# Kernel tuning notes

Measured on AMD Instinct MI355X. Metric: run time of the kernel, lower is better.

The kernel has to match this reference:

```python
import jax, jax.numpy as jnp
import numpy as np

N_NODES = 20000
N_EDGES = 320000
EMB = 256
K_DIFF = 3
BN_EPS = 1e-5


def conv1d(x, w, b, stride):
    # x: [N, Cin, L], w: [Cout, Cin, K]
    y = jax.lax.conv_general_dilated(x, w, window_strides=(stride,), padding='VALID',
                                     dimension_numbers=('NCH', 'OIH', 'NCH'))
    return y + b[None, :, None]


def batchnorm_train(x, gamma, beta):
    # training-mode BatchNorm1d over (N, L) per channel, biased variance
    m = jnp.mean(x, axis=(0, 2), keepdims=True)
    v = jnp.var(x, axis=(0, 2), keepdims=True)
    return (x - m) * jax.lax.rsqrt(v + BN_EPS) * gamma[None, :, None] + beta[None, :, None]


def dconv(X, W, b, row, col, norm_out, norm_in, n):
    # Diffusion convolution (pytorch_geometric_temporal DConv), K hops,
    # forward (out-degree) and backward (in-degree) random walks.
    def prop(x, norm):
        msg = norm[:, None] * x[row]                    # [E, F] gather
        return jax.ops.segment_sum(msg, col, num_segments=n)  # scatter-add to targets

    K = W.shape[1]
    Tx_0 = X
    Tx_1 = X
    H = X @ W[0, 0] + X @ W[1, 0]
    if K > 1:
        Tx_1_o = prop(X, norm_out)
        Tx_1_i = prop(X, norm_in)
        H = H + Tx_1_o @ W[0, 1] + Tx_1_i @ W[1, 1]
    for k in range(2, K):
        Tx_2_o = 2.0 * prop(Tx_1_o, norm_out) - Tx_0
        Tx_2_i = 2.0 * prop(Tx_1_i, norm_in) - Tx_0
        H = H + Tx_2_o @ W[0, k] + Tx_2_i @ W[1, k]
        Tx_0, Tx_1_o, Tx_1_i = Tx_1, Tx_2_o, Tx_2_i
    return H + b


def setup_inputs() -> dict:
    key = jax.random.key(0)
    ks = jax.random.split(key, 16)
    d_in = 2 * EMB  # concat([X, H])
    inp = {
        'x': jax.random.normal(ks[0], (N_NODES, 1, 100), dtype=jnp.float32),
        'edge_index': jax.random.randint(ks[1], (2, N_EDGES), 0, N_NODES, dtype=jnp.int32),
        'hidden_state': jax.random.normal(ks[2], (N_NODES, EMB), dtype=jnp.float32),
        'conv1_w': jax.random.normal(ks[3], (32, 1, 10), dtype=jnp.float32) * 0.2,
        'conv1_b': jnp.zeros((32,), jnp.float32),
        'bn1_gamma': jnp.ones((32,), jnp.float32),
        'bn1_beta': jnp.zeros((32,), jnp.float32),
        'conv2_w': jax.random.normal(ks[4], (32, 32, 10), dtype=jnp.float32) * 0.05,
        'conv2_b': jnp.zeros((32,), jnp.float32),
        'bn2_gamma': jnp.ones((32,), jnp.float32),
        'bn2_beta': jnp.zeros((32,), jnp.float32),
        'W_z': jax.random.normal(ks[5], (2, K_DIFF, d_in, EMB), dtype=jnp.float32) * 0.05,
        'b_z': jnp.zeros((EMB,), jnp.float32),
        'W_r': jax.random.normal(ks[6], (2, K_DIFF, d_in, EMB), dtype=jnp.float32) * 0.05,
        'b_r': jnp.zeros((EMB,), jnp.float32),
        'W_h': jax.random.normal(ks[7], (2, K_DIFF, d_in, EMB), dtype=jnp.float32) * 0.05,
        'b_h': jnp.zeros((EMB,), jnp.float32),
    }
    return inp


def reference(x, edge_index, hidden_state, conv1_w, conv1_b, bn1_gamma, bn1_beta,
              conv2_w, conv2_b, bn2_gamma, bn2_beta, W_z, b_z, W_r, b_r, W_h, b_h):
    n = x.shape[0]
    # CNN embedding: conv -> relu -> bn, twice
    h = batchnorm_train(jax.nn.relu(conv1d(x, conv1_w, conv1_b, 3)), bn1_gamma, bn1_beta)
    h = batchnorm_train(jax.nn.relu(conv1d(h, conv2_w, conv2_b, 3)), bn2_gamma, bn2_beta)
    X = h.reshape(n, -1)  # [N, EMB]

    row, col = edge_index[0], edge_index[1]
    ones = jnp.ones((row.shape[0],), X.dtype)
    deg_out = jax.ops.segment_sum(ones, row, num_segments=n)
    deg_in = jax.ops.segment_sum(ones, col, num_segments=n)
    norm_out = (1.0 / deg_out)[row]
    norm_in = (1.0 / deg_in)[col]

    H0 = hidden_state
    XH = jnp.concatenate([X, H0], axis=1)
    Z = jax.nn.sigmoid(dconv(XH, W_z, b_z, row, col, norm_out, norm_in, n))
    R = jax.nn.sigmoid(dconv(XH, W_r, b_r, row, col, norm_out, norm_in, n))
    XRH = jnp.concatenate([X, R * H0], axis=1)
    H_tilde = jnp.tanh(dconv(XRH, W_h, b_h, row, col, norm_out, norm_in, n))
    H = Z * H0 + (1.0 - Z) * H_tilde
    return jax.nn.relu(H)
```

## Files before the change

kernel.cpp:

```cpp
#include <hip/hip_runtime.h>
#include <cstdint>
#include <cstddef>

#define NN 20000
#define NE 320000

typedef float f32x4 __attribute__((ext_vector_type(4)));
typedef short s16x8 __attribute__((ext_vector_type(8)));
typedef unsigned short us;

struct KBd { const us* p; int rs; int cs; };
struct KB10 { KBd b[10]; };

__device__ __forceinline__ us f2bf(float x){
    unsigned u = __float_as_uint(x);
    unsigned r = (u + 0x7fffu + ((u >> 16) & 1u)) >> 16;
    return (us)r;
}
__device__ __forceinline__ float bf2f(us s){
    return __uint_as_float(((unsigned)s) << 16);
}

__device__ __forceinline__ void gl16(const void* g, void* l){
    __builtin_amdgcn_global_load_lds((const __attribute__((address_space(1))) unsigned int*)g,
                                     (__attribute__((address_space(3))) unsigned int*)l, 16, 0, 0);
}

__device__ __forceinline__ void upd8(uint4 v, float w, float* ao, float* ai){
    float f0=__uint_as_float(v.x<<16), f1=__uint_as_float(v.x&0xffff0000u);
    float f2=__uint_as_float(v.y<<16), f3=__uint_as_float(v.y&0xffff0000u);
    float f4=__uint_as_float(v.z<<16), f5=__uint_as_float(v.z&0xffff0000u);
    float f6=__uint_as_float(v.w<<16), f7=__uint_as_float(v.w&0xffff0000u);
    ao[0]=fmaf(w,f0,ao[0]); ao[1]=fmaf(w,f1,ao[1]); ao[2]=fmaf(w,f2,ao[2]); ao[3]=fmaf(w,f3,ao[3]);
    ao[4]=fmaf(w,f4,ao[4]); ao[5]=fmaf(w,f5,ao[5]); ao[6]=fmaf(w,f6,ao[6]); ao[7]=fmaf(w,f7,ao[7]);
    ai[0]+=f0; ai[1]+=f1; ai[2]+=f2; ai[3]+=f3; ai[4]+=f4; ai[5]+=f5; ai[6]+=f6; ai[7]+=f7;
}
__device__ __forceinline__ void updw(uint4 v, float w, float* a){
    float f0=__uint_as_float(v.x<<16), f1=__uint_as_float(v.x&0xffff0000u);
    float f2=__uint_as_float(v.y<<16), f3=__uint_as_float(v.y&0xffff0000u);
    float f4=__uint_as_float(v.z<<16), f5=__uint_as_float(v.z&0xffff0000u);
    float f6=__uint_as_float(v.w<<16), f7=__uint_as_float(v.w&0xffff0000u);
    a[0]=fmaf(w,f0,a[0]); a[1]=fmaf(w,f1,a[1]); a[2]=fmaf(w,f2,a[2]); a[3]=fmaf(w,f3,a[3]);
    a[4]=fmaf(w,f4,a[4]); a[5]=fmaf(w,f5,a[5]); a[6]=fmaf(w,f6,a[6]); a[7]=fmaf(w,f7,a[7]);
}
__device__ __forceinline__ uint4 pack8(const float* a){
    uint4 r;
    r.x=((unsigned)f2bf(a[1])<<16)|f2bf(a[0]);
    r.y=((unsigned)f2bf(a[3])<<16)|f2bf(a[2]);
    r.z=((unsigned)f2bf(a[5])<<16)|f2bf(a[4]);
    r.w=((unsigned)f2bf(a[7])<<16)|f2bf(a[6]);
    return r;
}
__device__ __forceinline__ uint4 pack8s(const float* a, float s){
    uint4 r;
    r.x=((unsigned)f2bf(s*a[1])<<16)|f2bf(s*a[0]);
    r.y=((unsigned)f2bf(s*a[3])<<16)|f2bf(s*a[2]);
    r.z=((unsigned)f2bf(s*a[5])<<16)|f2bf(s*a[4]);
    r.w=((unsigned)f2bf(s*a[7])<<16)|f2bf(s*a[6]);
    return r;
}


__global__ void k_zero(uint32_t* p, int n){
    int i = blockIdx.x*256 + threadIdx.x;
    if(i < n) p[i] = 0u;
}

__global__ void k_degree(const int* __restrict__ ei, int* degout, int* degin){
    int e = blockIdx.x*256 + threadIdx.x;
    if(e < NE){
        atomicAdd(&degout[ei[e]], 1);
        atomicAdd(&degin[ei[NE+e]], 1);
    }
}

__global__ void k_scan(const int* __restrict__ degin, int* __restrict__ coloff,
                       float* __restrict__ invdegin){
    __shared__ int part[1024];
    int t = threadIdx.x;
    int base = t*20;
    int s = 0;
    for(int k=0;k<20;k++){ int i = base+k; if(i < NN) s += degin[i]; }
    part[t] = s;
    __syncthreads();
    for(int off=1; off<1024; off<<=1){
        int v = (t>=off) ? part[t-off] : 0;
        __syncthreads();
        part[t] += v;
        __syncthreads();
    }
    int run = (t>0) ? part[t-1] : 0;
    for(int k=0;k<20;k++){
        int i = base+k;
        if(i < NN){
            int d = degin[i];
            coloff[i] = run;
            run += d;
            invdegin[i] = (d>0) ? (1.0f/(float)d) : 0.0f;
        }
    }
    if(t==1023) coloff[NN] = part[1023];
}

__global__ void k_csr(const int* __restrict__ ei, const int* __restrict__ degout,
                      const int* __restrict__ coloff, int* cnt, int2* __restrict__ ew){
    int e = blockIdx.x*256 + threadIdx.x;
    if(e < NE){
        int r = ei[e], c = ei[NE+e];
        int pos = coloff[c] + atomicAdd(&cnt[c], 1);
        int2 v; v.x = r; v.y = __float_as_int(1.0f/(float)degout[r]);
        ew[pos] = v;
    }
}


__global__ void k_conv1(const float* __restrict__ x, const float* __restrict__ w1,
                        const float* __restrict__ b1, us* __restrict__ y1b){
    __shared__ float w[320];
    __shared__ float bb[32];
    int t = threadIdx.x;
    for(int i=t;i<320;i+=256) w[i] = w1[i];
    if(t < 32) bb[t] = b1[t];
    __syncthreads();
    int gid = blockIdx.x*256 + t;
    if(gid >= NN*31) return;
    int node = gid/31, p = gid - node*31;
    const float* xr = x + node*100 + 3*p;
    float xv[10];
    #pragma unroll
    for(int k=0;k<10;k++) xv[k] = xr[k];
    us* yo = y1b + (size_t)node*1024 + p;
    #pragma unroll
    for(int c=0;c<32;c++){
        float a = bb[c];
        #pragma unroll
        for(int k=0;k<10;k++) a = fmaf(w[c*10+k], xv[k], a);
        yo[c*32] = f2bf(fmaxf(a, 0.0f));
    }
    if(p == 0){
        #pragma unroll
        for(int c=0;c<32;c++) y1b[(size_t)node*1024 + c*32 + 31] = 0;
    }
}

template<int SLOTS, int PPC>
__global__ void k_chanstats_bf(const us* __restrict__ y, float* __restrict__ sq){
    int tid = blockIdx.x*blockDim.x + threadIdx.x;
    int slot = tid & (SLOTS-1);
    int node0 = tid / SLOTS;
    int nstride = (gridDim.x*blockDim.x) / SLOTS;
    int c = slot / PPC;
    float s = 0.f, q = 0.f;
    for(int n=node0; n<NN; n+=nstride){
        float v = bf2f(y[(size_t)n*SLOTS + slot]);
        s += v; q = fmaf(v, v, q);
    }
    #pragma unroll
    for(int m=PPC>>1; m>0; m>>=1){
        s += __shfl_xor(s, m);
        q += __shfl_xor(q, m);
    }
    if((threadIdx.x & (PPC-1)) == 0){
        atomicAdd(&sq[c], s);
        atomicAdd(&sq[32+c], q);
    }
}

__global__ void k_bnfin(const float* __restrict__ sq, const float* __restrict__ gamma,
                        const float* __restrict__ beta, float* __restrict__ scsh,
                        float inv_count){
    int c = threadIdx.x;
    if(c < 32){
        float m = sq[c]*inv_count;
        float v = sq[32+c]*inv_count - m*m;
        float sc = gamma[c]*rsqrtf(v + 1e-5f);
        scsh[c] = sc;
        scsh[32+c] = beta[c] - m*sc;
    }
}

__global__ void __launch_bounds__(256) k_conv2(const us* __restrict__ y1b,
                        const float* __restrict__ w2, const float* __restrict__ b2,
                        const float* __restrict__ scsh1, us* __restrict__ Xpre){
    __shared__ float wlds[10240];
    __shared__ float hlds[8*1040];
    int t = threadIdx.x;
    int node0 = blockIdx.x*8;
    #pragma unroll
    for(int j=0;j<40;j++){
        int idx = j*256 + t;
        int ck = idx>>5, c2 = idx&31;
        wlds[ck*32 + c2] = w2[c2*320 + ck];
    }
    #pragma unroll
    for(int j=0;j<32;j++){
        int idx = j*256 + t;
        int nl = idx>>10, i = idx&1023;
        int c = i>>5;
        hlds[nl*1040 + i] = fmaf(scsh1[c], bf2f(y1b[(size_t)(node0+nl)*1024 + i]), scsh1[32+c]);
    }
    __syncthreads();
    int nl = t>>5, c2 = t&31;
    int hbase = nl*1040;
    float acc[8];
    float b = b2[c2];
    #pragma unroll
    for(int p=0;p<8;p++) acc[p] = b;
    for(int c=0;c<32;c++){
        float wr[10];
        #pragma unroll
        for(int k=0;k<10;k++) wr[k] = wlds[(c*10+k)*32 + c2];
        float hv[32];
        #pragma unroll
        for(int q=0;q<8;q++){
            float4 v = *(const float4*)&hlds[hbase + c*32 + q*4];
            hv[q*4+0]=v.x; hv[q*4+1]=v.y; hv[q*4+2]=v.z; hv[q*4+3]=v.w;
        }
        #pragma unroll
        for(int p=0;p<8;p++){
            #pragma unroll
            for(int k=0;k<10;k++)
                acc[p] = fmaf(wr[k], hv[3*p+k], acc[p]);
        }
    }
    uint4 pk;
    pk.x = ((unsigned)f2bf(fmaxf(acc[1],0.f))<<16) | f2bf(fmaxf(acc[0],0.f));
    pk.y = ((unsigned)f2bf(fmaxf(acc[3],0.f))<<16) | f2bf(fmaxf(acc[2],0.f));
    pk.z = ((unsigned)f2bf(fmaxf(acc[5],0.f))<<16) | f2bf(fmaxf(acc[4],0.f));
    pk.w = ((unsigned)f2bf(fmaxf(acc[7],0.f))<<16) | f2bf(fmaxf(acc[6],0.f));
    *(uint4*)&Xpre[(size_t)(node0+nl)*256 + c2*8] = pk;
}

__global__ void __launch_bounds__(256) k_prep(const us* __restrict__ Xpre,
        const float* __restrict__ scsh, const float* __restrict__ h0,
        us* __restrict__ XHp){
    int node = blockIdx.x*4 + (threadIdx.x>>6);
    if(node >= NN) return;
    int lane = threadIdx.x & 63;
    int half = lane>>5, g = lane&31;
    uint4 o;
    if(half == 0){
        uint4 v = *(const uint4*)(Xpre + (size_t)node*256 + g*8);
        float sc = scsh[g], sh = scsh[32+g];
        float y[8];
        y[0]=fmaf(sc,__uint_as_float(v.x<<16),sh); y[1]=fmaf(sc,__uint_as_float(v.x&0xffff0000u),sh);
        y[2]=fmaf(sc,__uint_as_float(v.y<<16),sh); y[3]=fmaf(sc,__uint_as_float(v.y&0xffff0000u),sh);
        y[4]=fmaf(sc,__uint_as_float(v.z<<16),sh); y[5]=fmaf(sc,__uint_as_float(v.z&0xffff0000u),sh);
        y[6]=fmaf(sc,__uint_as_float(v.w<<16),sh); y[7]=fmaf(sc,__uint_as_float(v.w&0xffff0000u),sh);
        o = pack8(y);
    }else{
        float4 a = *(const float4*)(h0 + (size_t)node*256 + g*8);
        float4 b = *(const float4*)(h0 + (size_t)node*256 + g*8 + 4);
        float y[8] = {a.x,a.y,a.z,a.w,b.x,b.y,b.z,b.w};
        o = pack8(y);
    }
    *(uint4*)(XHp + (size_t)node*512 + (size_t)g*16 + half*8) = o;
}


__device__ __forceinline__ float weff_val(const float* W, int term, size_t base){
    const size_t S = 512*256;
    if(term==0)      return W[0*S+base] + W[3*S+base] - W[2*S+base] - W[5*S+base];
    else if(term==1) return W[1*S+base];
    else if(term==2) return W[4*S+base];
    else if(term==3) return 2.0f*W[2*S+base];
    else             return 2.0f*W[5*S+base];
}

__global__ void k_weff_zr_t(const float* __restrict__ Wz, const float* __restrict__ Wr,
                            us* __restrict__ Wt){
    int k = blockIdx.x*256 + threadIdx.x;
    int col = blockIdx.y;
    const float* W = (col < 256) ? Wz : Wr;
    int j = col & 255;
    int kb = k >> 8, rr = k & 255;
    size_t base = (size_t)((kb & 1)*256 + rr)*256 + j;
    Wt[(size_t)col*2560 + k] = f2bf(weff_val(W, kb>>1, base));
}

__global__ void k_weff_h_t(const float* __restrict__ Wh, us* __restrict__ Wt){
    int k = blockIdx.x*256 + threadIdx.x;
    int col = blockIdx.y;
    int kb = k >> 8, rr = k & 255;
    size_t base = (size_t)((kb & 1)*256 + rr)*256 + col;
    Wt[(size_t)col*2560 + k] = f2bf(weff_val(Wh, kb>>1, base));
}


__global__ void __launch_bounds__(256) k_prop1(const us* __restrict__ XHp,
        const int* __restrict__ coloff, const int2* __restrict__ ew,
        const float* __restrict__ invdeg, us* __restrict__ T1op, us* __restrict__ T1ip){
    int node = blockIdx.x*4 + (threadIdx.x>>6);
    if(node >= NN) return;
    int lane = threadIdx.x & 63;
    size_t lo = (size_t)(lane&31)*16 + (lane>>5)*8;
    int s = coloff[node], e = coloff[node+1];
    float ao[8]={0,0,0,0,0,0,0,0}, ai[8]={0,0,0,0,0,0,0,0};
    int j = s;
    for(; j+3 < e; j += 4){
        int2 e0=ew[j], e1=ew[j+1], e2=ew[j+2], e3=ew[j+3];
        uint4 v0=*(const uint4*)(XHp+(size_t)e0.x*512+lo);
        uint4 v1=*(const uint4*)(XHp+(size_t)e1.x*512+lo);
        uint4 v2=*(const uint4*)(XHp+(size_t)e2.x*512+lo);
        uint4 v3=*(const uint4*)(XHp+(size_t)e3.x*512+lo);
        upd8(v0,__int_as_float(e0.y),ao,ai);
        upd8(v1,__int_as_float(e1.y),ao,ai);
        upd8(v2,__int_as_float(e2.y),ao,ai);
        upd8(v3,__int_as_float(e3.y),ao,ai);
    }
    for(; j < e; j++){
        int2 ed = ew[j];
        uint4 v = *(const uint4*)(XHp+(size_t)ed.x*512+lo);
        upd8(v,__int_as_float(ed.y),ao,ai);
    }
    float wi = invdeg[node];
    *(uint4*)(T1op+(size_t)node*512+lo) = pack8(ao);
    *(uint4*)(T1ip+(size_t)node*512+lo) = pack8s(ai,wi);
}

__global__ void __launch_bounds__(256) k_prop2(const us* __restrict__ T1op,
        const us* __restrict__ T1ip,
        const int* __restrict__ coloff, const int2* __restrict__ ew,
        const float* __restrict__ invdeg, us* __restrict__ P2op, us* __restrict__ P2ip){
    int node = blockIdx.x*4 + (threadIdx.x>>6);
    if(node >= NN) return;
    int lane = threadIdx.x & 63;
    size_t lo = (size_t)(lane&31)*16 + (lane>>5)*8;
    int s = coloff[node], e = coloff[node+1];
    float ao[8]={0,0,0,0,0,0,0,0}, ai[8]={0,0,0,0,0,0,0,0};
    int j = s;
    for(; j+1 < e; j += 2){
        int2 e0=ew[j], e1=ew[j+1];
        size_t o0=(size_t)e0.x*512+lo, o1=(size_t)e1.x*512+lo;
        uint4 a0=*(const uint4*)(T1op+o0), b0=*(const uint4*)(T1ip+o0);
        uint4 a1=*(const uint4*)(T1op+o1), b1=*(const uint4*)(T1ip+o1);
        float one = 1.0f;
        updw(a0,__int_as_float(e0.y),ao); updw(b0,one,ai);
        updw(a1,__int_as_float(e1.y),ao); updw(b1,one,ai);
    }
    if(j < e){
        int2 ed = ew[j];
        size_t o0=(size_t)ed.x*512+lo;
        uint4 a0=*(const uint4*)(T1op+o0), b0=*(const uint4*)(T1ip+o0);
        updw(a0,__int_as_float(ed.y),ao); updw(b0,1.0f,ai);
    }
    float wi = invdeg[node];
    *(uint4*)(P2op+(size_t)node*512+lo) = pack8(ao);
    *(uint4*)(P2ip+(size_t)node*512+lo) = pack8s(ai,wi);
}

__global__ void __launch_bounds__(256) k_propq1(const us* __restrict__ RHb,
        const int* __restrict__ coloff, const int2* __restrict__ ew,
        const float* __restrict__ invdeg, us* __restrict__ Q1p){
    int node = blockIdx.x*4 + (threadIdx.x>>6);
    if(node >= NN) return;
    int lane = threadIdx.x & 63;
    int half = lane>>5, g = lane&31;
    int s = coloff[node], e = coloff[node+1];
    float ao[8]={0,0,0,0,0,0,0,0}, ai[8]={0,0,0,0,0,0,0,0};
    int j = s;
    for(; j+1 < e; j += 2){
        int2 ed = ew[j+half];
        uint4 v = *(const uint4*)(RHb+(size_t)ed.x*256+g*8);
        upd8(v,__int_as_float(ed.y),ao,ai);
    }
    if(j < e && half == 0){
        int2 ed = ew[j];
        uint4 v = *(const uint4*)(RHb+(size_t)ed.x*256+g*8);
        upd8(v,__int_as_float(ed.y),ao,ai);
    }
    #pragma unroll
    for(int k=0;k<8;k++){
        ao[k] += __shfl_xor(ao[k],32);
        ai[k] += __shfl_xor(ai[k],32);
    }
    if(half == 0){
        float wi = invdeg[node];
        *(uint4*)(Q1p+(size_t)node*512+(size_t)g*16)   = pack8(ao);
        *(uint4*)(Q1p+(size_t)node*512+(size_t)g*16+8) = pack8s(ai,wi);
    }
}

__global__ void __launch_bounds__(256) k_propq2(const us* __restrict__ Q1p,
        const int* __restrict__ coloff, const int2* __restrict__ ew,
        const float* __restrict__ invdeg, us* __restrict__ Q2p){
    int node = blockIdx.x*4 + (threadIdx.x>>6);
    if(node >= NN) return;
    int lane = threadIdx.x & 63;
    int half = lane>>5;
    size_t lo = (size_t)(lane&31)*16 + half*8;
    int s = coloff[node], e = coloff[node+1];
    float a[8]={0,0,0,0,0,0,0,0};
    int j = s;
    for(; j+3 < e; j += 4){
        int2 e0=ew[j], e1=ew[j+1], e2=ew[j+2], e3=ew[j+3];
        uint4 v0=*(const uint4*)(Q1p+(size_t)e0.x*512+lo);
        uint4 v1=*(const uint4*)(Q1p+(size_t)e1.x*512+lo);
        uint4 v2=*(const uint4*)(Q1p+(size_t)e2.x*512+lo);
        uint4 v3=*(const uint4*)(Q1p+(size_t)e3.x*512+lo);
        updw(v0, half ? 1.0f : __int_as_float(e0.y), a);
        updw(v1, half ? 1.0f : __int_as_float(e1.y), a);
        updw(v2, half ? 1.0f : __int_as_float(e2.y), a);
        updw(v3, half ? 1.0f : __int_as_float(e3.y), a);
    }
    for(; j < e; j++){
        int2 ed = ew[j];
        uint4 v = *(const uint4*)(Q1p+(size_t)ed.x*512+lo);
        updw(v, half ? 1.0f : __int_as_float(ed.y), a);
    }
    float sc = half ? invdeg[node] : 1.0f;
    *(uint4*)(Q2p+(size_t)node*512+lo) = pack8s(a,sc);
}


template<int MODE, int BNT>
__global__ void __launch_bounds__(256) k_gemm(KB10 blocks, const us* __restrict__ Wt,
        const float* __restrict__ bias0, const float* __restrict__ bias1,
        const float* __restrict__ h0, const float* __restrict__ Zin,
        float* __restrict__ out0, us* __restrict__ out1){
    constexpr int WN = BNT/32;
    constexpr int NB = BNT/64;
    __shared__ us As[2][4096];
    __shared__ us Bs[2][BNT*32];
    int t = threadIdx.x;
    int wid = t >> 6, lane = t & 63;
    int l15 = lane & 15, kg = lane >> 4;

    int bid = blockIdx.x;
    int xcd = bid & 7, sblk = bid >> 3;
    int cidx = sblk & 3, r = (sblk >> 2)*8 + xcd;
    if(r >= 157) return;
    int row0 = r*128, col0 = cidx*BNT;
    int rowbase = (wid >> 1)*64, colbase = (wid & 1)*(BNT/2);
    int swz = (l15 >> 1) & 3;

    int srA[2], sgA[2], graA[2];
    #pragma unroll
    for(int i=0;i<2;i++){
        int c = t + i*256;
        srA[i] = c >> 2;
        sgA[i] = (c & 3) ^ ((srA[i] >> 1) & 3);
        int gr = row0 + srA[i];
        graA[i] = (gr < NN) ? gr : NN-1;
    }
    int srB[NB], sgB[NB];
    #pragma unroll
    for(int i=0;i<NB;i++){
        int c = t + i*256;
        srB[i] = c >> 2;
        sgB[i] = (c & 3) ^ ((srB[i] >> 1) & 3);
    }

    f32x4 acc[4][WN] = {};

    auto stage = [&](int buf, int step){
        int kb = step >> 3, kt = (step & 7)*32, ktc = (step & 7)*4;
        const us* Ap = blocks.b[kb].p;
        int rs = blocks.b[kb].rs, cs = blocks.b[kb].cs;
        #pragma unroll
        for(int i=0;i<2;i++)
            gl16(Ap + (size_t)graA[i]*rs + (size_t)(ktc + sgA[i])*cs, &As[buf][(t+i*256)*8]);
        const us* Wp = Wt + (size_t)kb*256;
        #pragma unroll
        for(int i=0;i<NB;i++)
            gl16(Wp + (size_t)(col0+srB[i])*2560 + kt + sgB[i]*8, &Bs[buf][(t+i*256)*8]);
    };

    stage(0, 0);
    __syncthreads();
    int cur = 0;
    for(int step=0; step<80; step++){
        if(step < 79) stage(cur^1, step+1);
        s16x8 af[4], bfr[WN];
        #pragma unroll
        for(int i=0;i<4;i++){
            int row = rowbase + i*16 + l15;
            af[i] = *(const s16x8*)&As[cur][(row*4 + (kg ^ swz))*8];
        }
        #pragma unroll
        for(int n=0;n<WN;n++){
            int colr = colbase + n*16 + l15;
            bfr[n] = *(const s16x8*)&Bs[cur][(colr*4 + (kg ^ swz))*8];
        }
        #pragma unroll
        for(int mi=0;mi<4;mi++){
            #pragma unroll
            for(int ni=0;ni<WN;ni++){
                acc[mi][ni] = __builtin_amdgcn_mfma_f32_16x16x32_bf16(
                    af[mi], bfr[ni], acc[mi][ni], 0, 0, 0);
            }
        }
        __syncthreads();
        cur ^= 1;
    }

    #pragma unroll
    for(int mi=0;mi<4;mi++){
        int gr0 = row0 + rowbase + mi*16 + kg*4;
        #pragma unroll
        for(int ni=0;ni<WN;ni++){
            int j = col0 + colbase + ni*16 + l15;
            #pragma unroll
            for(int rr=0;rr<4;rr++){
                int gr = gr0 + rr;
                if(gr < NN){
                    float a = acc[mi][ni][rr];
                    if(MODE == 0){
                        if(j < 256){
                            out0[(size_t)gr*256 + j] = 1.0f/(1.0f + expf(-(a + bias0[j])));
                        }else{
                            int jj = j - 256;
                            float rv = 1.0f/(1.0f + expf(-(a + bias1[jj])));
                            out1[(size_t)gr*256 + jj] = f2bf(rv * h0[(size_t)gr*256 + jj]);
                        }
                    }else{
                        float z = Zin[(size_t)gr*256 + j];
                        float ht = tanhf(a + bias0[j]);
                        float H = z*h0[(size_t)gr*256 + j] + (1.0f - z)*ht;
                        out0[(size_t)gr*256 + j] = fmaxf(H, 0.0f);
                    }
                }
            }
        }
    }
}


extern "C" void kernel_launch(void* const* d_in, const int* in_sizes, int n_in,
                              void* d_out, int out_size, void* d_ws, size_t ws_size,
                              hipStream_t stream){
    const float* x   = (const float*)d_in[0];
    const int*   ei  = (const int*)  d_in[1];
    const float* h0  = (const float*)d_in[2];
    const float* w1  = (const float*)d_in[3];
    const float* b1  = (const float*)d_in[4];
    const float* g1  = (const float*)d_in[5];
    const float* be1 = (const float*)d_in[6];
    const float* w2  = (const float*)d_in[7];
    const float* b2  = (const float*)d_in[8];
    const float* g2  = (const float*)d_in[9];
    const float* be2 = (const float*)d_in[10];
    const float* Wz  = (const float*)d_in[11];
    const float* bz  = (const float*)d_in[12];
    const float* Wr  = (const float*)d_in[13];
    const float* br  = (const float*)d_in[14];
    const float* Wh  = (const float*)d_in[15];
    const float* bh  = (const float*)d_in[16];
    float* out = (float*)d_out;
    float* wsf = (float*)d_ws;
    (void)in_sizes; (void)n_in; (void)out_size;

    const size_t O_DEGO=0, O_DEGI=20000, O_CNT=40000, O_BN=60000;
    const size_t O_COLOFF=60288, O_EW=80384, O_INVDEG=720384;
    const size_t O_WTZR=740480, O_WTH=1395840;
    const size_t O_XPRE=1723520;
    const size_t O_XHP=4283520;
    const size_t O_T1OP=9403520, O_T1IP=14523520, O_P2OP=19643520, O_P2IP=24763520;
    const size_t O_Q1P=29883520, O_Q2P=35003520;
    const size_t O_RH=40123520, O_Z=42683520;
    const size_t WS_NEED_BYTES = (size_t)47803520 * 4;
    if(ws_size < WS_NEED_BYTES) return;

    int* degout = (int*)(wsf + O_DEGO);
    int* degin  = (int*)(wsf + O_DEGI);
    int* cnt    = (int*)(wsf + O_CNT);
    float* bn   = wsf + O_BN;
    int* coloff = (int*)(wsf + O_COLOFF);
    int2* ew    = (int2*)(wsf + O_EW);
    float* invdeg = wsf + O_INVDEG;
    us* Wtzr = (us*)(wsf + O_WTZR);
    us* Wth  = (us*)(wsf + O_WTH);
    us* Xpre = (us*)(wsf + O_XPRE);
    us* XHp  = (us*)(wsf + O_XHP);
    us* T1op = (us*)(wsf + O_T1OP);
    us* T1ip = (us*)(wsf + O_T1IP);
    us* P2op = (us*)(wsf + O_P2OP);
    us* P2ip = (us*)(wsf + O_P2IP);
    us* Q1p  = (us*)(wsf + O_Q1P);
    us* Q2p  = (us*)(wsf + O_Q2P);
    us* RHb  = (us*)(wsf + O_RH);
    float* Z = wsf + O_Z;
    us* y1b  = (us*)(wsf + O_T1OP);

    k_zero<<<236,256,0,stream>>>((uint32_t*)(wsf + O_DEGO), 60256);
    k_degree<<<1250,256,0,stream>>>(ei, degout, degin);
    k_scan<<<1,1024,0,stream>>>(degin, coloff, invdeg);
    k_csr<<<1250,256,0,stream>>>(ei, degout, coloff, cnt, ew);

    k_conv1<<<2422,256,0,stream>>>(x, w1, b1, y1b);
    k_chanstats_bf<1024,32><<<256,256,0,stream>>>(y1b, bn+0);
    k_bnfin<<<1,32,0,stream>>>(bn+0, g1, be1, bn+64, 1.0f/620000.0f);
    k_conv2<<<2500,256,0,stream>>>(y1b, w2, b2, bn+64, Xpre);
    k_chanstats_bf<256,8><<<64,256,0,stream>>>(Xpre, bn+128);
    k_bnfin<<<1,32,0,stream>>>(bn+128, g2, be2, bn+192, 1.0f/160000.0f);
    k_prep<<<5000,256,0,stream>>>(Xpre, bn+192, h0, XHp);

    k_weff_zr_t<<<dim3(10,512),256,0,stream>>>(Wz, Wr, Wtzr);
    k_weff_h_t<<<dim3(10,256),256,0,stream>>>(Wh, Wth);

    k_prop1<<<5000,256,0,stream>>>(XHp, coloff, ew, invdeg, T1op, T1ip);
    k_prop2<<<5000,256,0,stream>>>(T1op, T1ip, coloff, ew, invdeg, P2op, P2ip);

    KB10 bzr = {{ {XHp,512,16},{XHp+8,512,16},{T1op,512,16},{T1op+8,512,16},
                  {T1ip,512,16},{T1ip+8,512,16},{P2op,512,16},{P2op+8,512,16},
                  {P2ip,512,16},{P2ip+8,512,16} }};
    k_gemm<0,128><<<640,256,0,stream>>>(bzr, Wtzr, bz, br, h0, nullptr, Z, RHb);

    k_propq1<<<5000,256,0,stream>>>(RHb, coloff, ew, invdeg, Q1p);
    k_propq2<<<5000,256,0,stream>>>(Q1p, coloff, ew, invdeg, Q2p);

    KB10 bhh = {{ {XHp,512,16},{RHb,256,8},{T1op,512,16},{Q1p,512,16},
                  {T1ip,512,16},{Q1p+8,512,16},{P2op,512,16},{Q2p,512,16},
                  {P2ip,512,16},{Q2p+8,512,16} }};
    k_gemm<1,64><<<640,256,0,stream>>>(bhh, Wth, bh, nullptr, h0, Z, out, nullptr);
}
```

Before: 791.7 us.

## Triple-stage GEMM pipeline, contiguous operand buffers, deeper gather unrolls, unified propagation kernel

The GEMM prologue now issues two stages ahead and uses explicit vmcnt waits and raw barriers instead of __syncthreads, so global-to-LDS loads overlap MFMA work. Operand buffers are laid out contiguously with a fixed stride, so A addresses come from simple arithmetic instead of a struct of pointers. The R*H output is written duplicated into a 512-wide interleaved layout, which lets the first Q propagation reuse the generic k_propu kernel. The gather loops in prop1, prop2 and propu are unrolled deeper to keep more loads in flight. The risks are that the hand-tuned waitcnt values must match the exact number of loads per stage, the deeper unrolls raise register pressure, and the duplicated RH layout doubles that buffer's traffic.

```diff
diff --git a/kernel.cpp b/kernel.cpp
--- a/kernel.cpp
+++ b/kernel.cpp
@@ -4,13 +4,11 @@
 
 #define NN 20000
 #define NE 320000
+#define SBUF 10240000
 
 typedef float f32x4 __attribute__((ext_vector_type(4)));
 typedef short s16x8 __attribute__((ext_vector_type(8)));
 typedef unsigned short us;
-
-struct KBd { const us* p; int rs; int cs; };
-struct KB10 { KBd b[10]; };
 
 __device__ __forceinline__ us f2bf(float x){
     unsigned u = __float_as_uint(x);
@@ -297,21 +295,19 @@
     int s = coloff[node], e = coloff[node+1];
     float ao[8]={0,0,0,0,0,0,0,0}, ai[8]={0,0,0,0,0,0,0,0};
     int j = s;
-    for(; j+3 < e; j += 4){
-        int2 e0=ew[j], e1=ew[j+1], e2=ew[j+2], e3=ew[j+3];
-        uint4 v0=*(const uint4*)(XHp+(size_t)e0.x*512+lo);
-        uint4 v1=*(const uint4*)(XHp+(size_t)e1.x*512+lo);
-        uint4 v2=*(const uint4*)(XHp+(size_t)e2.x*512+lo);
-        uint4 v3=*(const uint4*)(XHp+(size_t)e3.x*512+lo);
-        upd8(v0,__int_as_float(e0.y),ao,ai);
-        upd8(v1,__int_as_float(e1.y),ao,ai);
-        upd8(v2,__int_as_float(e2.y),ao,ai);
-        upd8(v3,__int_as_float(e3.y),ao,ai);
+    for(; j+7 < e; j += 8){
+        int2 ed[8]; uint4 v[8];
+        #pragma unroll
+        for(int i=0;i<8;i++) ed[i] = ew[j+i];
+        #pragma unroll
+        for(int i=0;i<8;i++) v[i] = *(const uint4*)(XHp+(size_t)ed[i].x*512+lo);
+        #pragma unroll
+        for(int i=0;i<8;i++) upd8(v[i], __int_as_float(ed[i].y), ao, ai);
     }
     for(; j < e; j++){
         int2 ed = ew[j];
         uint4 v = *(const uint4*)(XHp+(size_t)ed.x*512+lo);
-        upd8(v,__int_as_float(ed.y),ao,ai);
+        upd8(v, __int_as_float(ed.y), ao, ai);
     }
     float wi = invdeg[node];
     *(uint4*)(T1op+(size_t)node*512+lo) = pack8(ao);
@@ -329,61 +325,36 @@
     int s = coloff[node], e = coloff[node+1];
     float ao[8]={0,0,0,0,0,0,0,0}, ai[8]={0,0,0,0,0,0,0,0};
     int j = s;
-    for(; j+1 < e; j += 2){
-        int2 e0=ew[j], e1=ew[j+1];
-        size_t o0=(size_t)e0.x*512+lo, o1=(size_t)e1.x*512+lo;
-        uint4 a0=*(const uint4*)(T1op+o0), b0=*(const uint4*)(T1ip+o0);
-        uint4 a1=*(const uint4*)(T1op+o1), b1=*(const uint4*)(T1ip+o1);
-        float one = 1.0f;
-        updw(a0,__int_as_float(e0.y),ao); updw(b0,one,ai);
-        updw(a1,__int_as_float(e1.y),ao); updw(b1,one,ai);
-    }
-    if(j < e){
+    for(; j+3 < e; j += 4){
+        int2 ed[4]; uint4 va[4], vb[4];
+        #pragma unroll
+        for(int i=0;i<4;i++) ed[i] = ew[j+i];
+        #pragma unroll
+        for(int i=0;i<4;i++){
+            size_t o = (size_t)ed[i].x*512+lo;
+            va[i] = *(const uint4*)(T1op+o);
+            vb[i] = *(const uint4*)(T1ip+o);
+        }
+        #pragma unroll
+        for(int i=0;i<4;i++){
+            updw(va[i], __int_as_float(ed[i].y), ao);
+            updw(vb[i], 1.0f, ai);
+        }
+    }
+    for(; j < e; j++){
         int2 ed = ew[j];
-        size_t o0=(size_t)ed.x*512+lo;
-        uint4 a0=*(const uint4*)(T1op+o0), b0=*(const uint4*)(T1ip+o0);
-        updw(a0,__int_as_float(ed.y),ao); updw(b0,1.0f,ai);
+        size_t o = (size_t)ed.x*512+lo;
+        updw(*(const uint4*)(T1op+o), __int_as_float(ed.y), ao);
+        updw(*(const uint4*)(T1ip+o), 1.0f, ai);
     }
     float wi = invdeg[node];
     *(uint4*)(P2op+(size_t)node*512+lo) = pack8(ao);
     *(uint4*)(P2ip+(size_t)node*512+lo) = pack8s(ai,wi);
 }
 
-__global__ void __launch_bounds__(256) k_propq1(const us* __restrict__ RHb,
+__global__ void __launch_bounds__(256) k_propu(const us* __restrict__ Yin,
         const int* __restrict__ coloff, const int2* __restrict__ ew,
-        const float* __restrict__ invdeg, us* __restrict__ Q1p){
-    int node = blockIdx.x*4 + (threadIdx.x>>6);
-    if(node >= NN) return;
-    int lane = threadIdx.x & 63;
-    int half = lane>>5, g = lane&31;
-    int s = coloff[node], e = coloff[node+1];
-    float ao[8]={0,0,0,0,0,0,0,0}, ai[8]={0,0,0,0,0,0,0,0};
-    int j = s;
-    for(; j+1 < e; j += 2){
-        int2 ed = ew[j+half];
-        uint4 v = *(const uint4*)(RHb+(size_t)ed.x*256+g*8);
-        upd8(v,__int_as_float(ed.y),ao,ai);
-    }
-    if(j < e && half == 0){
-        int2 ed = ew[j];
-        uint4 v = *(const uint4*)(RHb+(size_t)ed.x*256+g*8);
-        upd8(v,__int_as_float(ed.y),ao,ai);
-    }
-    #pragma unroll
-    for(int k=0;k<8;k++){
-        ao[k] += __shfl_xor(ao[k],32);
-        ai[k] += __shfl_xor(ai[k],32);
-    }
-    if(half == 0){
-        float wi = invdeg[node];
-        *(uint4*)(Q1p+(size_t)node*512+(size_t)g*16)   = pack8(ao);
-        *(uint4*)(Q1p+(size_t)node*512+(size_t)g*16+8) = pack8s(ai,wi);
-    }
-}
-
-__global__ void __launch_bounds__(256) k_propq2(const us* __restrict__ Q1p,
-        const int* __restrict__ coloff, const int2* __restrict__ ew,
-        const float* __restrict__ invdeg, us* __restrict__ Q2p){
+        const float* __restrict__ invdeg, us* __restrict__ Pout){
     int node = blockIdx.x*4 + (threadIdx.x>>6);
     if(node >= NN) return;
     int lane = threadIdx.x & 63;
@@ -392,29 +363,28 @@
     int s = coloff[node], e = coloff[node+1];
     float a[8]={0,0,0,0,0,0,0,0};
     int j = s;
-    for(; j+3 < e; j += 4){
-        int2 e0=ew[j], e1=ew[j+1], e2=ew[j+2], e3=ew[j+3];
-        uint4 v0=*(const uint4*)(Q1p+(size_t)e0.x*512+lo);
-        uint4 v1=*(const uint4*)(Q1p+(size_t)e1.x*512+lo);
-        uint4 v2=*(const uint4*)(Q1p+(size_t)e2.x*512+lo);
-        uint4 v3=*(const uint4*)(Q1p+(size_t)e3.x*512+lo);
-        updw(v0, half ? 1.0f : __int_as_float(e0.y), a);
-        updw(v1, half ? 1.0f : __int_as_float(e1.y), a);
-        updw(v2, half ? 1.0f : __int_as_float(e2.y), a);
-        updw(v3, half ? 1.0f : __int_as_float(e3.y), a);
+    for(; j+7 < e; j += 8){
+        int2 ed[8]; uint4 v[8];
+        #pragma unroll
+        for(int i=0;i<8;i++) ed[i] = ew[j+i];
+        #pragma unroll
+        for(int i=0;i<8;i++) v[i] = *(const uint4*)(Yin+(size_t)ed[i].x*512+lo);
+        #pragma unroll
+        for(int i=0;i<8;i++) updw(v[i], half ? 1.0f : __int_as_float(ed[i].y), a);
     }
     for(; j < e; j++){
         int2 ed = ew[j];
-        uint4 v = *(const uint4*)(Q1p+(size_t)ed.x*512+lo);
+        uint4 v = *(const uint4*)(Yin+(size_t)ed.x*512+lo);
         updw(v, half ? 1.0f : __int_as_float(ed.y), a);
     }
     float sc = half ? invdeg[node] : 1.0f;
-    *(uint4*)(Q2p+(size_t)node*512+lo) = pack8s(a,sc);
+    *(uint4*)(Pout+(size_t)node*512+lo) = pack8s(a,sc);
 }
 
 
 template<int MODE, int BNT>
-__global__ void __launch_bounds__(256) k_gemm(KB10 blocks, const us* __restrict__ Wt,
+__global__ void __launch_bounds__(256) k_gemm(const us* __restrict__ XG,
+        const us* __restrict__ RG, const us* __restrict__ Wt,
         const float* __restrict__ bias0, const float* __restrict__ bias1,
         const float* __restrict__ h0, const float* __restrict__ Zin,
         float* __restrict__ out0, us* __restrict__ out1){
@@ -434,43 +404,59 @@
     int rowbase = (wid >> 1)*64, colbase = (wid & 1)*(BNT/2);
     int swz = (l15 >> 1) & 3;
 
-    int srA[2], sgA[2], graA[2];
+    int srA[2], sgA[2];
+    size_t rowoffA[2];
     #pragma unroll
     for(int i=0;i<2;i++){
         int c = t + i*256;
         srA[i] = c >> 2;
         sgA[i] = (c & 3) ^ ((srA[i] >> 1) & 3);
         int gr = row0 + srA[i];
-        graA[i] = (gr < NN) ? gr : NN-1;
+        gr = (gr < NN) ? gr : NN-1;
+        rowoffA[i] = (size_t)gr*512 + (size_t)sgA[i]*16;
     }
     int srB[NB], sgB[NB];
+    size_t coloffB[NB];
     #pragma unroll
     for(int i=0;i<NB;i++){
         int c = t + i*256;
         srB[i] = c >> 2;
         sgB[i] = (c & 3) ^ ((srB[i] >> 1) & 3);
+        coloffB[i] = (size_t)(col0+srB[i])*2560 + (size_t)sgB[i]*8;
     }
 
     f32x4 acc[4][WN] = {};
 
-    auto stage = [&](int buf, int step){
-        int kb = step >> 3, kt = (step & 7)*32, ktc = (step & 7)*4;
-        const us* Ap = blocks.b[kb].p;
-        int rs = blocks.b[kb].rs, cs = blocks.b[kb].cs;
+    auto stage = [&](int buf, int s){
+        int kb = s >> 3;
+        int ktc = (s & 7) * 4;
+        const us* Ap;
+        if(MODE == 0){
+            Ap = XG + (size_t)(kb >> 1) * SBUF + (size_t)(kb & 1) * 8;
+        }else{
+            if((kb & 1) == 0) Ap = XG + (size_t)(kb >> 1) * SBUF;
+            else Ap = RG + (size_t)((kb + 1) >> 2) * SBUF + (size_t)(((kb + 1) >> 1) & 1) * 8;
+        }
         #pragma unroll
         for(int i=0;i<2;i++)
-            gl16(Ap + (size_t)graA[i]*rs + (size_t)(ktc + sgA[i])*cs, &As[buf][(t+i*256)*8]);
-        const us* Wp = Wt + (size_t)kb*256;
+            gl16(Ap + rowoffA[i] + (size_t)ktc*16, &As[buf][(t+i*256)*8]);
+        const us* Wp = Wt + (size_t)kb*256 + (s & 7)*32;
         #pragma unroll
         for(int i=0;i<NB;i++)
-            gl16(Wp + (size_t)(col0+srB[i])*2560 + kt + sgB[i]*8, &Bs[buf][(t+i*256)*8]);
+            gl16(Wp + coloffB[i], &Bs[buf][(t+i*256)*8]);
     };
 
     stage(0, 0);
-    __syncthreads();
-    int cur = 0;
-    for(int step=0; step<80; step++){
-        if(step < 79) stage(cur^1, step+1);
+    stage(1, 1);
+    for(int step=0; step<80; ++step){
+        int cur = step & 1;
+        if(step < 79){
+            if(MODE == 0) asm volatile("s_waitcnt vmcnt(4)" ::: "memory");
+            else          asm volatile("s_waitcnt vmcnt(3)" ::: "memory");
+        }else{
+            asm volatile("s_waitcnt vmcnt(0)" ::: "memory");
+        }
+        __builtin_amdgcn_s_barrier();
         s16x8 af[4], bfr[WN];
         #pragma unroll
         for(int i=0;i<4;i++){
@@ -482,6 +468,11 @@
             int colr = colbase + n*16 + l15;
             bfr[n] = *(const s16x8*)&Bs[cur][(colr*4 + (kg ^ swz))*8];
         }
+        asm volatile("s_waitcnt lgkmcnt(0)" ::: "memory");
+        __builtin_amdgcn_sched_barrier(0);
+        __builtin_amdgcn_s_barrier();
+        if(step < 78) stage(cur, step+2);
+        __builtin_amdgcn_s_setprio(1);
         #pragma unroll
         for(int mi=0;mi<4;mi++){
             #pragma unroll
@@ -490,8 +481,7 @@
                     af[mi], bfr[ni], acc[mi][ni], 0, 0, 0);
             }
         }
-        __syncthreads();
-        cur ^= 1;
+        __builtin_amdgcn_s_setprio(0);
     }
 
     #pragma unroll
@@ -511,7 +501,10 @@
                         }else{
                             int jj = j - 256;
                             float rv = 1.0f/(1.0f + expf(-(a + bias1[jj])));
-                            out1[(size_t)gr*256 + jj] = f2bf(rv * h0[(size_t)gr*256 + jj]);
+                            us v = f2bf(rv * h0[(size_t)gr*256 + jj]);
+                            size_t base = (size_t)gr*512 + (size_t)(jj>>3)*16 + (jj&7);
+                            out1[base] = v;
+                            out1[base+8] = v;
                         }
                     }else{
                         float z = Zin[(size_t)gr*256 + j];
@@ -554,12 +547,13 @@
     const size_t O_COLOFF=60288, O_EW=80384, O_INVDEG=720384;
     const size_t O_WTZR=740480, O_WTH=1395840;
     const size_t O_XPRE=1723520;
-    const size_t O_XHP=4283520;
-    const size_t O_T1OP=9403520, O_T1IP=14523520, O_P2OP=19643520, O_P2IP=24763520;
-    const size_t O_Q1P=29883520, O_Q2P=35003520;
-    const size_t O_RH=40123520, O_Z=42683520;
-    const size_t WS_NEED_BYTES = (size_t)47803520 * 4;
+    const size_t O_XG=4283520;
+    const size_t O_RG=29883520;
+    const size_t O_Z=45243520;
+    const size_t WS_NEED_BYTES = (size_t)50363520 * 4;
     if(ws_size < WS_NEED_BYTES) return;
+
+    const size_t SW = 5120000;
 
     int* degout = (int*)(wsf + O_DEGO);
     int* degin  = (int*)(wsf + O_DEGI);
@@ -571,16 +565,18 @@
     us* Wtzr = (us*)(wsf + O_WTZR);
     us* Wth  = (us*)(wsf + O_WTH);
     us* Xpre = (us*)(wsf + O_XPRE);
-    us* XHp  = (us*)(wsf + O_XHP);
-    us* T1op = (us*)(wsf + O_T1OP);
-    us* T1ip = (us*)(wsf + O_T1IP);
-    us* P2op = (us*)(wsf + O_P2OP);
-    us* P2ip = (us*)(wsf + O_P2IP);
-    us* Q1p  = (us*)(wsf + O_Q1P);
-    us* Q2p  = (us*)(wsf + O_Q2P);
-    us* RHb  = (us*)(wsf + O_RH);
+    us* XG   = (us*)(wsf + O_XG);
+    us* RG   = (us*)(wsf + O_RG);
+    us* XHp  = XG;
+    us* T1op = (us*)(wsf + O_XG + SW);
+    us* T1ip = (us*)(wsf + O_XG + 2*SW);
+    us* P2op = (us*)(wsf + O_XG + 3*SW);
+    us* P2ip = (us*)(wsf + O_XG + 4*SW);
+    us* RHp  = RG;
+    us* Q1p  = (us*)(wsf + O_RG + SW);
+    us* Q2p  = (us*)(wsf + O_RG + 2*SW);
     float* Z = wsf + O_Z;
-    us* y1b  = (us*)(wsf + O_T1OP);
+    us* y1b  = T1op;
 
     k_zero<<<236,256,0,stream>>>((uint32_t*)(wsf + O_DEGO), 60256);
     k_degree<<<1250,256,0,stream>>>(ei, degout, degin);
@@ -601,16 +597,10 @@
     k_prop1<<<5000,256,0,stream>>>(XHp, coloff, ew, invdeg, T1op, T1ip);
     k_prop2<<<5000,256,0,stream>>>(T1op, T1ip, coloff, ew, invdeg, P2op, P2ip);
 
-    KB10 bzr = {{ {XHp,512,16},{XHp+8,512,16},{T1op,512,16},{T1op+8,512,16},
-                  {T1ip,512,16},{T1ip+8,512,16},{P2op,512,16},{P2op+8,512,16},
-                  {P2ip,512,16},{P2ip+8,512,16} }};
-    k_gemm<0,128><<<640,256,0,stream>>>(bzr, Wtzr, bz, br, h0, nullptr, Z, RHb);
-
-    k_propq1<<<5000,256,0,stream>>>(RHb, coloff, ew, invdeg, Q1p);
-    k_propq2<<<5000,256,0,stream>>>(Q1p, coloff, ew, invdeg, Q2p);
-
-    KB10 bhh = {{ {XHp,512,16},{RHb,256,8},{T1op,512,16},{Q1p,512,16},
-                  {T1ip,512,16},{Q1p+8,512,16},{P2op,512,16},{Q2p,512,16},
-                  {P2ip,512,16},{Q2p+8,512,16} }};
-    k_gemm<1,64><<<640,256,0,stream>>>(bhh, Wth, bh, nullptr, h0, Z, out, nullptr);
-}
+    k_gemm<0,128><<<640,256,0,stream>>>(XG, RG, Wtzr, bz, br, h0, nullptr, Z, RHp);
+
+    k_propu<<<5000,256,0,stream>>>(RHp, coloff, ew, invdeg, Q1p);
+    k_propu<<<5000,256,0,stream>>>(Q1p, coloff, ew, invdeg, Q2p);
+
+    k_gemm<1,64><<<640,256,0,stream>>>(XG, RG, Wth, bh, nullptr, h0, Z, out, nullptr);
+}
```

New measurement: 793.0 us. No clear change (+0.2%).
